# Kernel optimization log

Hardware: AMD Instinct MI355X
Metric: run time of the kernel (lower is better)

Reference implementation:

```python
import jax, jax.numpy as jnp
import numpy as np

LAMBDA = 0.2
BETA = 1.0
EPS = 1e-6


def setup_inputs() -> dict:
    key = jax.random.key(0)
    t_prime = jax.random.normal(key, (8192, 768), dtype=jnp.float32)
    return {"t_prime": t_prime}


def reference(t_prime) -> jnp.ndarray:
    vocab = t_prime.shape[0]
    # L2-normalize rows (matches F.normalize p=2, dim=1 with its 1e-12 clamp)
    norm = jnp.maximum(jnp.linalg.norm(t_prime, axis=1, keepdims=True), 1e-12)
    t_norm = t_prime / norm
    # [vocab, vocab] cosine similarity
    S = t_norm @ t_norm.T
    diag = jnp.diagonal(S)
    collapse = jnp.sum((diag - 1.0) ** 2)
    # HNS path: off-diagonal entries per row, expressed without boolean reshape.
    # neg_sims = S with diagonal removed; reweight * neg^2 = beta * neg^3 / (mean_neg + eps)
    S_off = S - jnp.diag(diag)  # zero diagonal == off-diagonal values
    mean_neg = jnp.sum(S_off, axis=1) / (vocab - 1)  # per-row mean of negatives
    row_cube = jnp.sum(S_off ** 3, axis=1)  # diagonal contributes 0
    hard_neg_loss = BETA * jnp.sum(row_cube / (mean_neg + EPS))
    return collapse + LAMBDA * hard_neg_loss
```

## Files before the change

kernel.cpp:

```cpp
#include <hip/hip_runtime.h>
#include <math.h>

#define VV 8192
#define DD 768
#define NDMAX 256

typedef __attribute__((ext_vector_type(8))) short bf16x8;
typedef __attribute__((ext_vector_type(4))) float f32x4;

__device__ inline ushort f2bf(float f) {
    uint u = __float_as_uint(f);
    uint r = (u + 0x7fffu + ((u >> 16) & 1u)) >> 16;
    return (ushort)r;
}
__device__ inline float bf2f(ushort h) { return __uint_as_float(((uint)h) << 16); }

__device__ inline void gload16(const ushort* g, ushort* l) {
    __builtin_amdgcn_global_load_lds(
        (const __attribute__((address_space(1))) void*)g,
        (__attribute__((address_space(3))) void*)l, 16, 0, 0);
}

__global__ __launch_bounds__(256) void k_normpack(const float* __restrict__ t,
                                                  float* __restrict__ norms,
                                                  ushort* __restrict__ xh,
                                                  ushort* __restrict__ xl,
                                                  float* __restrict__ rc,
                                                  int* __restrict__ dlist,
                                                  int* __restrict__ dcount) {
    int r = blockIdx.x;
    const float* tr = t + (size_t)r * DD;
    int tid = threadIdx.x;
    float v0 = tr[tid], v1 = tr[tid + 256], v2 = tr[tid + 512];
    double s = (double)v0 * v0 + (double)v1 * v1 + (double)v2 * v2;
#pragma unroll
    for (int o = 32; o > 0; o >>= 1) s += __shfl_down(s, o, 64);
    __shared__ double wsum[4];
    int lane = tid & 63, w = tid >> 6;
    if (lane == 0) wsum[w] = s;
    __syncthreads();
    double tot = wsum[0] + wsum[1] + wsum[2] + wsum[3];
    float norm = fmaxf((float)sqrt(tot), 1e-12f);
    if (tid == 0) {
        norms[r] = norm;
        rc[r] = 0.f;
    }
    if (r == 0) {
        dlist[tid] = -1;
        if (tid == 0) *dcount = 0;
    }
    size_t base = (size_t)r * DD;
#pragma unroll
    for (int q = 0; q < 3; ++q) {
        int k = tid + q * 256;
        float v = (q == 0 ? v0 : (q == 1 ? v1 : v2)) / norm;
        ushort h = f2bf(v);
        xh[base + k] = h;
        xl[base + k] = f2bf(v - bf2f(h));
    }
}

__global__ __launch_bounds__(256) void k_colsumA(const float* __restrict__ t,
                                                 const float* __restrict__ norms,
                                                 double* __restrict__ gp) {
    int k = threadIdx.x;
    int r0 = blockIdx.x * 32;
    double s0 = 0.0, s1 = 0.0, s2 = 0.0;
    for (int r = r0; r < r0 + 32; ++r) {
        const float* tr = t + (size_t)r * DD;
        float nrm = norms[r];
        s0 += (double)(tr[k] / nrm);
        s1 += (double)(tr[k + 256] / nrm);
        s2 += (double)(tr[k + 512] / nrm);
    }
    double* gb = gp + (size_t)blockIdx.x * DD;
    gb[k] = s0;
    gb[k + 256] = s1;
    gb[k + 512] = s2;
}

__global__ __launch_bounds__(256) void k_colsumB(const double* __restrict__ gp,
                                                 double* __restrict__ g) {
    int col = blockIdx.x * 256 + threadIdx.x;
    double s = 0.0;
    for (int b = 0; b < 256; ++b) s += gp[(size_t)b * DD + col];
    g[col] = s;
}

__global__ __launch_bounds__(256) void k_mean(const float* __restrict__ t,
                                              const float* __restrict__ norms,
                                              const double* __restrict__ g,
                                              double* __restrict__ mnum,
                                              double* __restrict__ dd,
                                              int* __restrict__ dlist,
                                              int* __restrict__ dcount) {
    int r = blockIdx.x * 4 + (threadIdx.x >> 6);
    int lane = threadIdx.x & 63;
    const float* tr = t + (size_t)r * DD;
    float nrm = norms[r];
    double xg = 0.0, xx = 0.0;
#pragma unroll
    for (int k = lane; k < DD; k += 64) {
        float xf = tr[k] / nrm;
        double xv = (double)xf;
        xg += xv * g[k];
        xx += xv * xv;
    }
#pragma unroll
    for (int o = 32; o > 0; o >>= 1) {
        xg += __shfl_down(xg, o, 64);
        xx += __shfl_down(xx, o, 64);
    }
    if (lane == 0) {
        double m = xg - xx;
        mnum[r] = m;
        dd[r] = xx;
        if (fabs(m / 8191.0 + 1e-6) < 1e-5) {
            int pos = atomicAdd(dcount, 1);
            if (pos < NDMAX) dlist[pos] = r;
        }
    }
}

__global__ __launch_bounds__(256, 3) void k_cube(const ushort* __restrict__ xh,
                                                 const ushort* __restrict__ xl,
                                                 const int* __restrict__ dlist,
                                                 float* __restrict__ Sb,
                                                 float* __restrict__ rc) {
    __shared__ ushort As0[4096], As1[4096], As2[4096];
    __shared__ ushort Bs0[4096], Bs1[4096], Bs2[4096];

    const int bid = blockIdx.x;
    const int tid = threadIdx.x;
    const int lane = tid & 63;
    const int wid = tid >> 6;
    const int l15 = lane & 15, li4 = lane >> 4;
    const int wm = wid >> 1, wn = wid & 1;

    const bool strip = (bid < 384);
    int bi = 0, bj = 0, seg = 0, rp = 0, cp = 0;
    if (strip) {
        seg = bid >> 7;
        int rem = bid & 127;
        rp = rem >> 6;
        cp = rem & 63;
    } else {
        int idx = bid - 384;
        int wg = (idx & 7) * 260 + (idx >> 3);
        int b = 0, cnt = 484;
        while (wg >= cnt) { wg -= cnt; ++b; cnt -= 64; }
        int cc = 0, h = 1;
        while (wg >= h) { wg -= h; ++cc; h = (cc < 7) ? cc + 1 : 8; }
        bi = 8 * b + wg;
        bj = 8 * b + cc;
    }
    const ushort* XA = strip ? ((seg == 1) ? xl : xh) : xh;
    const ushort* XB = strip ? ((seg == 2) ? xl : xh) : xh;

    int asrc[2], bsrc[2], ldst[2];
#pragma unroll
    for (int j = 0; j < 2; ++j) {
        int li = tid + j * 256;
        int row = li >> 2;
        int sl = ((li & 3) ^ ((li >> 3) & 3)) * 8;
        int ar = strip ? dlist[rp * 128 + row] : (bi * 128 + row);
        if (ar < 0) ar = 0;
        int br = strip ? (cp * 128 + row) : (bj * 128 + row);
        asrc[j] = ar * DD + sl;
        bsrc[j] = br * DD + sl;
        ldst[j] = li * 8;
    }

    const int swz = (li4 ^ ((l15 >> 1) & 3)) << 3;
    const int aoff = (wm * 64 + l15) * 32 + swz;
    const int boff = (wn * 64 + l15) * 32 + swz;

    f32x4 acc[4][4];
#pragma unroll
    for (int f = 0; f < 4; ++f)
#pragma unroll
        for (int n = 0; n < 4; ++n) acc[f][n] = (f32x4){0.f, 0.f, 0.f, 0.f};

#define STG(AW, BW, KT)                                  \
    do {                                                 \
        const int kq_ = (KT) * 32;                       \
        gload16(XA + asrc[0] + kq_, (AW) + ldst[0]);     \
        gload16(XB + bsrc[0] + kq_, (BW) + ldst[0]);     \
        gload16(XA + asrc[1] + kq_, (AW) + ldst[1]);     \
        gload16(XB + bsrc[1] + kq_, (BW) + ldst[1]);     \
    } while (0)

#define COMPUTE(AR, BR)                                                     \
    do {                                                                    \
        bf16x8 av[4], bv[4];                                                \
        _Pragma("unroll") for (int f = 0; f < 4; ++f) {                     \
            av[f] = *(const bf16x8*)((AR) + aoff + f * 512);                \
            bv[f] = *(const bf16x8*)((BR) + boff + f * 512);                \
        }                                                                   \
        _Pragma("unroll") for (int f = 0; f < 4; ++f)                       \
            _Pragma("unroll") for (int n = 0; n < 4; ++n)                   \
                acc[f][n] = __builtin_amdgcn_mfma_f32_16x16x32_bf16(        \
                    av[f], bv[n], acc[f][n], 0, 0, 0);                      \
    } while (0)

#define VMW4() asm volatile("s_waitcnt vmcnt(4)" ::: "memory")
#define VMW0() asm volatile("s_waitcnt vmcnt(0)" ::: "memory")
#define RBAR() asm volatile("s_barrier" ::: "memory")

    STG(As0, Bs0, 0);
    STG(As1, Bs1, 1);
    VMW4(); RBAR();

    for (int tb = 0; tb < 21; tb += 3) {
        STG(As2, Bs2, tb + 2);
        COMPUTE(As0, Bs0);
        VMW4(); RBAR();
        STG(As0, Bs0, tb + 3);
        COMPUTE(As1, Bs1);
        VMW4(); RBAR();
        STG(As1, Bs1, tb + 4);
        COMPUTE(As2, Bs2);
        VMW4(); RBAR();
    }
    STG(As2, Bs2, 23);
    COMPUTE(As0, Bs0);
    VMW4(); RBAR();
    COMPUTE(As1, Bs1);
    VMW0(); RBAR();
    COMPUTE(As2, Bs2);
#undef STG
#undef COMPUTE
#undef VMW4
#undef VMW0
#undef RBAR

    if (strip) {
#pragma unroll
        for (int f = 0; f < 4; ++f)
#pragma unroll
            for (int n = 0; n < 4; ++n)
#pragma unroll
                for (int r = 0; r < 4; ++r) {
                    int slot = seg * 256 + rp * 128 + wm * 64 + f * 16 + li4 * 4 + r;
                    int col = cp * 128 + wn * 64 + n * 16 + l15;
                    Sb[((size_t)slot << 13) + col] = acc[f][n][r];
                }
        return;
    }

    const bool dblk = (bi == bj);
    const int R0 = bi * 128, C0 = bj * 128;
    float rsum[4][4], csum[4];
#pragma unroll
    for (int n = 0; n < 4; ++n) csum[n] = 0.f;
#pragma unroll
    for (int f = 0; f < 4; ++f)
#pragma unroll
        for (int r = 0; r < 4; ++r) rsum[f][r] = 0.f;
#pragma unroll
    for (int f = 0; f < 4; ++f)
#pragma unroll
        for (int n = 0; n < 4; ++n)
#pragma unroll
            for (int r = 0; r < 4; ++r) {
                float s = acc[f][n][r];
                float c = s * s * s;
                int ri = wm * 64 + f * 16 + li4 * 4 + r;
                int cj = wn * 64 + n * 16 + l15;
                if (dblk && ri == cj) c = 0.f;
                rsum[f][r] += c;
                csum[n] += c;
            }
#pragma unroll
    for (int o = 1; o < 16; o <<= 1)
#pragma unroll
        for (int f = 0; f < 4; ++f)
#pragma unroll
            for (int r = 0; r < 4; ++r)
                rsum[f][r] += __shfl_xor(rsum[f][r], o, 64);
    if (l15 == 0) {
#pragma unroll
        for (int f = 0; f < 4; ++f)
#pragma unroll
            for (int r = 0; r < 4; ++r)
                atomicAdd(&rc[R0 + wm * 64 + f * 16 + li4 * 4 + r], rsum[f][r]);
    }
    if (!dblk) {
#pragma unroll
        for (int o = 16; o < 64; o <<= 1)
#pragma unroll
            for (int n = 0; n < 4; ++n) csum[n] += __shfl_xor(csum[n], o, 64);
        if (li4 == 0) {
#pragma unroll
            for (int n = 0; n < 4; ++n)
                atomicAdd(&rc[C0 + wn * 64 + n * 16 + l15], csum[n]);
        }
    }
}

__global__ __launch_bounds__(256) void k_cubefin(const float* __restrict__ Sb,
                                                 const int* __restrict__ dlist,
                                                 float* __restrict__ rc) {
    const int slot = blockIdx.x;
    const int drow = dlist[slot];
    if (drow < 0) return;
    const int tid = threadIdx.x;
    const float* s0p = Sb + ((size_t)slot << 13);
    const float* s1p = Sb + ((size_t)(256 + slot) << 13);
    const float* s2p = Sb + ((size_t)(512 + slot) << 13);
    float sum = 0.f;
    for (int c = tid; c < VV; c += 256) {
        float s0 = s0p[c];
        float sf = s0 + s1p[c] + s2p[c];
        float d = sf * sf * sf - s0 * s0 * s0;
        if (c == drow) d = 0.f;
        sum += d;
    }
    __shared__ float red[256];
    red[tid] = sum;
    __syncthreads();
    for (int o = 128; o > 0; o >>= 1) {
        if (tid < o) red[tid] += red[tid + o];
        __syncthreads();
    }
    if (tid == 0) atomicAdd(&rc[drow], red[0]);
}

__global__ __launch_bounds__(256) void k_final(const float* __restrict__ rc,
                                               const double* __restrict__ mnum,
                                               const double* __restrict__ dd,
                                               float* __restrict__ out) {
    int tid = threadIdx.x;
    double acc = 0.0, col = 0.0;
    for (int r = tid; r < VV; r += 256) {
        double m = mnum[r] / 8191.0 + 1e-6;
        acc += (double)rc[r] / m;
        double dm = dd[r] - 1.0;
        col += dm * dm;
    }
    __shared__ double sa[256], sc[256];
    sa[tid] = acc;
    sc[tid] = col;
    __syncthreads();
    for (int o = 128; o > 0; o >>= 1) {
        if (tid < o) {
            sa[tid] += sa[tid + o];
            sc[tid] += sc[tid + o];
        }
        __syncthreads();
    }
    if (tid == 0) out[0] = (float)(sc[0] + 0.2 * sa[0]);
}

extern "C" void kernel_launch(void* const* d_in, const int* in_sizes, int n_in,
                              void* d_out, int out_size, void* d_ws, size_t ws_size,
                              hipStream_t stream) {
    const float* t = (const float*)d_in[0];
    float* out = (float*)d_out;

    char* ws = (char*)d_ws;
    float* Sb = (float*)ws;
    size_t off = (size_t)VV * DD * sizeof(float);
    ushort* xh = (ushort*)(ws + off); off += (size_t)VV * DD * sizeof(ushort);
    ushort* xl = (ushort*)(ws + off); off += (size_t)VV * DD * sizeof(ushort);
    double* g = (double*)(ws + off);  off += DD * sizeof(double);
    double* mnum = (double*)(ws + off); off += VV * sizeof(double);
    double* dd = (double*)(ws + off);  off += VV * sizeof(double);
    float* rc = (float*)(ws + off);    off += VV * sizeof(float);
    int* dlist = (int*)(ws + off);     off += NDMAX * sizeof(int);
    int* dcount = (int*)(ws + off);    off += sizeof(int) + 60;
    float* norms = (float*)(ws + off); off += VV * sizeof(float);
    double* gp = (double*)(ws + off);  off += (size_t)256 * DD * sizeof(double);

    k_normpack<<<VV, 256, 0, stream>>>(t, norms, xh, xl, rc, dlist, dcount);
    k_colsumA<<<256, 256, 0, stream>>>(t, norms, gp);
    k_colsumB<<<3, 256, 0, stream>>>(gp, g);
    k_mean<<<VV / 4, 256, 0, stream>>>(t, norms, g, mnum, dd, dlist, dcount);
    k_cube<<<2464, 256, 0, stream>>>(xh, xl, dlist, Sb, rc);
    k_cubefin<<<NDMAX, 256, 0, stream>>>(Sb, dlist, rc);
    k_final<<<1, 256, 0, stream>>>(rc, mnum, dd, out);
}
```

Before: 142.5 us.

## Widen cube GEMM tiles to 128x256 and parallelize small reductions

The symmetric Gram/cube kernel moves from 128x128 tiles to 128x256 tiles, so each block does twice the MFMA work per A-tile load. The triangular tile enumeration and diagonal masking are rewritten for the new shape, the strip blocks for the degenerate rows are halved, and occupancy drops to 2 blocks per CU because of the larger LDS buffers and accumulators. The column-sum reduction kernel now splits its work across 24 blocks with a shared-memory reduction, and the final reduction runs with 1024 threads. The wider tiles cut redundant loads but add register pressure and compute slightly more of the redundant region near the diagonal.

```diff
diff --git a/kernel.cpp b/kernel.cpp
--- a/kernel.cpp
+++ b/kernel.cpp
@@ -81,10 +81,19 @@
 
 __global__ __launch_bounds__(256) void k_colsumB(const double* __restrict__ gp,
                                                  double* __restrict__ g) {
-    int col = blockIdx.x * 256 + threadIdx.x;
+    __shared__ double red[8][32];
+    int c = threadIdx.x & 31, part = threadIdx.x >> 5;
+    int col = blockIdx.x * 32 + c;
     double s = 0.0;
-    for (int b = 0; b < 256; ++b) s += gp[(size_t)b * DD + col];
-    g[col] = s;
+    for (int b = part * 32; b < part * 32 + 32; ++b)
+        s += gp[(size_t)b * DD + col];
+    red[part][c] = s;
+    __syncthreads();
+    if (part == 0) {
+        double tt = 0.0;
+        for (int p = 0; p < 8; ++p) tt += red[p][c];
+        g[col] = tt;
+    }
 }
 
 __global__ __launch_bounds__(256) void k_mean(const float* __restrict__ t,
@@ -122,13 +131,13 @@
     }
 }
 
-__global__ __launch_bounds__(256, 3) void k_cube(const ushort* __restrict__ xh,
+__global__ __launch_bounds__(256, 2) void k_cube(const ushort* __restrict__ xh,
                                                  const ushort* __restrict__ xl,
                                                  const int* __restrict__ dlist,
                                                  float* __restrict__ Sb,
                                                  float* __restrict__ rc) {
     __shared__ ushort As0[4096], As1[4096], As2[4096];
-    __shared__ ushort Bs0[4096], Bs1[4096], Bs2[4096];
+    __shared__ ushort Bs0[8192], Bs1[8192], Bs2[8192];
 
     const int bid = blockIdx.x;
     const int tid = threadIdx.x;
@@ -137,27 +146,25 @@
     const int l15 = lane & 15, li4 = lane >> 4;
     const int wm = wid >> 1, wn = wid & 1;
 
-    const bool strip = (bid < 384);
+    const bool strip = (bid < 192);
     int bi = 0, bj = 0, seg = 0, rp = 0, cp = 0;
     if (strip) {
-        seg = bid >> 7;
-        int rem = bid & 127;
-        rp = rem >> 6;
-        cp = rem & 63;
+        seg = bid >> 6;
+        int rem = bid & 63;
+        rp = rem >> 5;
+        cp = rem & 31;
     } else {
-        int idx = bid - 384;
-        int wg = (idx & 7) * 260 + (idx >> 3);
-        int b = 0, cnt = 484;
-        while (wg >= cnt) { wg -= cnt; ++b; cnt -= 64; }
-        int cc = 0, h = 1;
-        while (wg >= h) { wg -= h; ++cc; h = (cc < 7) ? cc + 1 : 8; }
-        bi = 8 * b + wg;
-        bj = 8 * b + cc;
+        int idx = bid - 192;
+        int wg = (idx & 7) * 132 + (idx >> 3);
+        int j = 0;
+        while (wg >= 2 * j + 2) { wg -= 2 * j + 2; ++j; }
+        bi = wg;
+        bj = j;
     }
     const ushort* XA = strip ? ((seg == 1) ? xl : xh) : xh;
     const ushort* XB = strip ? ((seg == 2) ? xl : xh) : xh;
 
-    int asrc[2], bsrc[2], ldst[2];
+    int asrc[2], bsrc[4], lda_[2], ldb_[4];
 #pragma unroll
     for (int j = 0; j < 2; ++j) {
         int li = tid + j * 256;
@@ -165,72 +172,81 @@
         int sl = ((li & 3) ^ ((li >> 3) & 3)) * 8;
         int ar = strip ? dlist[rp * 128 + row] : (bi * 128 + row);
         if (ar < 0) ar = 0;
-        int br = strip ? (cp * 128 + row) : (bj * 128 + row);
         asrc[j] = ar * DD + sl;
+        lda_[j] = li * 8;
+    }
+#pragma unroll
+    for (int j = 0; j < 4; ++j) {
+        int li = tid + j * 256;
+        int row = li >> 2;
+        int sl = ((li & 3) ^ ((li >> 3) & 3)) * 8;
+        int br = strip ? (cp * 256 + row) : (bj * 256 + row);
         bsrc[j] = br * DD + sl;
-        ldst[j] = li * 8;
+        ldb_[j] = li * 8;
     }
 
     const int swz = (li4 ^ ((l15 >> 1) & 3)) << 3;
     const int aoff = (wm * 64 + l15) * 32 + swz;
-    const int boff = (wn * 64 + l15) * 32 + swz;
-
-    f32x4 acc[4][4];
+    const int boff = (wn * 128 + l15) * 32 + swz;
+
+    f32x4 acc[4][8];
 #pragma unroll
     for (int f = 0; f < 4; ++f)
 #pragma unroll
-        for (int n = 0; n < 4; ++n) acc[f][n] = (f32x4){0.f, 0.f, 0.f, 0.f};
+        for (int n = 0; n < 8; ++n) acc[f][n] = (f32x4){0.f, 0.f, 0.f, 0.f};
 
 #define STG(AW, BW, KT)                                  \
     do {                                                 \
         const int kq_ = (KT) * 32;                       \
-        gload16(XA + asrc[0] + kq_, (AW) + ldst[0]);     \
-        gload16(XB + bsrc[0] + kq_, (BW) + ldst[0]);     \
-        gload16(XA + asrc[1] + kq_, (AW) + ldst[1]);     \
-        gload16(XB + bsrc[1] + kq_, (BW) + ldst[1]);     \
+        gload16(XA + asrc[0] + kq_, (AW) + lda_[0]);     \
+        gload16(XA + asrc[1] + kq_, (AW) + lda_[1]);     \
+        gload16(XB + bsrc[0] + kq_, (BW) + ldb_[0]);     \
+        gload16(XB + bsrc[1] + kq_, (BW) + ldb_[1]);     \
+        gload16(XB + bsrc[2] + kq_, (BW) + ldb_[2]);     \
+        gload16(XB + bsrc[3] + kq_, (BW) + ldb_[3]);     \
     } while (0)
 
 #define COMPUTE(AR, BR)                                                     \
     do {                                                                    \
-        bf16x8 av[4], bv[4];                                                \
-        _Pragma("unroll") for (int f = 0; f < 4; ++f) {                     \
+        bf16x8 av[4], bv[8];                                                \
+        _Pragma("unroll") for (int f = 0; f < 4; ++f)                       \
             av[f] = *(const bf16x8*)((AR) + aoff + f * 512);                \
-            bv[f] = *(const bf16x8*)((BR) + boff + f * 512);                \
-        }                                                                   \
+        _Pragma("unroll") for (int n = 0; n < 8; ++n)                       \
+            bv[n] = *(const bf16x8*)((BR) + boff + n * 512);                \
         _Pragma("unroll") for (int f = 0; f < 4; ++f)                       \
-            _Pragma("unroll") for (int n = 0; n < 4; ++n)                   \
+            _Pragma("unroll") for (int n = 0; n < 8; ++n)                   \
                 acc[f][n] = __builtin_amdgcn_mfma_f32_16x16x32_bf16(        \
                     av[f], bv[n], acc[f][n], 0, 0, 0);                      \
     } while (0)
 
-#define VMW4() asm volatile("s_waitcnt vmcnt(4)" ::: "memory")
+#define VMW6() asm volatile("s_waitcnt vmcnt(6)" ::: "memory")
 #define VMW0() asm volatile("s_waitcnt vmcnt(0)" ::: "memory")
 #define RBAR() asm volatile("s_barrier" ::: "memory")
 
     STG(As0, Bs0, 0);
     STG(As1, Bs1, 1);
-    VMW4(); RBAR();
+    VMW6(); RBAR();
 
     for (int tb = 0; tb < 21; tb += 3) {
         STG(As2, Bs2, tb + 2);
         COMPUTE(As0, Bs0);
-        VMW4(); RBAR();
+        VMW6(); RBAR();
         STG(As0, Bs0, tb + 3);
         COMPUTE(As1, Bs1);
-        VMW4(); RBAR();
+        VMW6(); RBAR();
         STG(As1, Bs1, tb + 4);
         COMPUTE(As2, Bs2);
-        VMW4(); RBAR();
+        VMW6(); RBAR();
     }
     STG(As2, Bs2, 23);
     COMPUTE(As0, Bs0);
-    VMW4(); RBAR();
+    VMW6(); RBAR();
     COMPUTE(As1, Bs1);
     VMW0(); RBAR();
     COMPUTE(As2, Bs2);
 #undef STG
 #undef COMPUTE
-#undef VMW4
+#undef VMW6
 #undef VMW0
 #undef RBAR
 
@@ -238,21 +254,21 @@
 #pragma unroll
         for (int f = 0; f < 4; ++f)
 #pragma unroll
-            for (int n = 0; n < 4; ++n)
+            for (int n = 0; n < 8; ++n)
 #pragma unroll
                 for (int r = 0; r < 4; ++r) {
                     int slot = seg * 256 + rp * 128 + wm * 64 + f * 16 + li4 * 4 + r;
-                    int col = cp * 128 + wn * 64 + n * 16 + l15;
+                    int col = cp * 256 + wn * 128 + n * 16 + l15;
                     Sb[((size_t)slot << 13) + col] = acc[f][n][r];
                 }
         return;
     }
 
-    const bool dblk = (bi == bj);
-    const int R0 = bi * 128, C0 = bj * 128;
-    float rsum[4][4], csum[4];
-#pragma unroll
-    for (int n = 0; n < 4; ++n) csum[n] = 0.f;
+    const bool dtile = ((bi >> 1) == bj);
+    const int R0 = bi * 128, C0 = bj * 256;
+    float rsum[4][4], csum[8];
+#pragma unroll
+    for (int n = 0; n < 8; ++n) csum[n] = 0.f;
 #pragma unroll
     for (int f = 0; f < 4; ++f)
 #pragma unroll
@@ -260,14 +276,14 @@
 #pragma unroll
     for (int f = 0; f < 4; ++f)
 #pragma unroll
-        for (int n = 0; n < 4; ++n)
+        for (int n = 0; n < 8; ++n)
 #pragma unroll
             for (int r = 0; r < 4; ++r) {
                 float s = acc[f][n][r];
                 float c = s * s * s;
-                int ri = wm * 64 + f * 16 + li4 * 4 + r;
-                int cj = wn * 64 + n * 16 + l15;
-                if (dblk && ri == cj) c = 0.f;
+                int ri = R0 + wm * 64 + f * 16 + li4 * 4 + r;
+                int cj = C0 + wn * 128 + n * 16 + l15;
+                if (dtile && ri == cj) c = 0.f;
                 rsum[f][r] += c;
                 csum[n] += c;
             }
@@ -285,15 +301,15 @@
             for (int r = 0; r < 4; ++r)
                 atomicAdd(&rc[R0 + wm * 64 + f * 16 + li4 * 4 + r], rsum[f][r]);
     }
-    if (!dblk) {
+    if (!dtile) {
 #pragma unroll
         for (int o = 16; o < 64; o <<= 1)
 #pragma unroll
-            for (int n = 0; n < 4; ++n) csum[n] += __shfl_xor(csum[n], o, 64);
+            for (int n = 0; n < 8; ++n) csum[n] += __shfl_xor(csum[n], o, 64);
         if (li4 == 0) {
 #pragma unroll
-            for (int n = 0; n < 4; ++n)
-                atomicAdd(&rc[C0 + wn * 64 + n * 16 + l15], csum[n]);
+            for (int n = 0; n < 8; ++n)
+                atomicAdd(&rc[C0 + wn * 128 + n * 16 + l15], csum[n]);
         }
     }
 }
@@ -326,23 +342,23 @@
     if (tid == 0) atomicAdd(&rc[drow], red[0]);
 }
 
-__global__ __launch_bounds__(256) void k_final(const float* __restrict__ rc,
-                                               const double* __restrict__ mnum,
-                                               const double* __restrict__ dd,
-                                               float* __restrict__ out) {
+__global__ __launch_bounds__(1024) void k_final(const float* __restrict__ rc,
+                                                const double* __restrict__ mnum,
+                                                const double* __restrict__ dd,
+                                                float* __restrict__ out) {
     int tid = threadIdx.x;
     double acc = 0.0, col = 0.0;
-    for (int r = tid; r < VV; r += 256) {
+    for (int r = tid; r < VV; r += 1024) {
         double m = mnum[r] / 8191.0 + 1e-6;
         acc += (double)rc[r] / m;
         double dm = dd[r] - 1.0;
         col += dm * dm;
     }
-    __shared__ double sa[256], sc[256];
+    __shared__ double sa[1024], sc[1024];
     sa[tid] = acc;
     sc[tid] = col;
     __syncthreads();
-    for (int o = 128; o > 0; o >>= 1) {
+    for (int o = 512; o > 0; o >>= 1) {
         if (tid < o) {
             sa[tid] += sa[tid + o];
             sc[tid] += sc[tid + o];
@@ -374,9 +390,9 @@
 
     k_normpack<<<VV, 256, 0, stream>>>(t, norms, xh, xl, rc, dlist, dcount);
     k_colsumA<<<256, 256, 0, stream>>>(t, norms, gp);
-    k_colsumB<<<3, 256, 0, stream>>>(gp, g);
+    k_colsumB<<<24, 256, 0, stream>>>(gp, g);
     k_mean<<<VV / 4, 256, 0, stream>>>(t, norms, g, mnum, dd, dlist, dcount);
-    k_cube<<<2464, 256, 0, stream>>>(xh, xl, dlist, Sb, rc);
+    k_cube<<<1248, 256, 0, stream>>>(xh, xl, dlist, Sb, rc);
     k_cubefin<<<NDMAX, 256, 0, stream>>>(Sb, dlist, rc);
-    k_final<<<1, 256, 0, stream>>>(rc, mnum, dd, out);
-}
+    k_final<<<1, 1024, 0, stream>>>(rc, mnum, dd, out);
+}
```

Measured after the change: 133.5 us. -6.3%, faster.
